# Kernel optimization log

Measured on AMD Instinct MI355X. Metric: run time of the kernel, lower is better.

The kernel has to match this reference:

```python
import jax, jax.numpy as jnp
import numpy as np

K = 8            # NEAREST_K
IN = 68          # input_size = 64 + 4
EO = 32          # edge_output_size
FEAT = IN * 2 + EO * 4  # 264
EMB = 32         # linear_embedding
NCLS = 2
N = 768
EPS = 1e-5


def lrelu(x):
    return jnp.where(x >= 0, x, 0.01 * x)


def setup_inputs() -> dict:
    key = jax.random.key(0)
    ks = jax.random.split(key, 16)

    def w(k, fan_in, fan_out):
        return jax.random.normal(k, (fan_in, fan_out), jnp.float32) / np.float32(np.sqrt(fan_in))

    return {
        "feat0": jax.random.normal(ks[0], (N, IN), jnp.float32),
        "feat1": jax.random.normal(ks[1], (N, IN), jnp.float32),
        # edge_conv1: Linear(IN*K, EO) -> LeakyReLU -> Linear(EO, EO) -> LeakyReLU
        "ec1_w1": w(ks[2], IN * K, EO), "ec1_b1": jnp.zeros((EO,), jnp.float32),
        "ec1_w2": w(ks[3], EO, EO),     "ec1_b2": jnp.zeros((EO,), jnp.float32),
        # edge_conv2: Linear(EO*K, EO) -> LeakyReLU -> Linear(EO, EO) -> LeakyReLU
        "ec2_w1": w(ks[4], EO * K, EO), "ec2_b1": jnp.zeros((EO,), jnp.float32),
        "ec2_w2": w(ks[5], EO, EO),     "ec2_b2": jnp.zeros((EO,), jnp.float32),
        # linear head: BN(FEAT) -> Linear(FEAT,EMB) -> LReLU -> Linear(EMB,EMB) -> LReLU -> Linear(EMB,NCLS)
        "bn_g": jnp.ones((FEAT,), jnp.float32), "bn_b": jnp.zeros((FEAT,), jnp.float32),
        "lin1_w": w(ks[6], FEAT, EMB), "lin1_b": jnp.zeros((EMB,), jnp.float32),
        "lin2_w": w(ks[7], EMB, EMB),  "lin2_b": jnp.zeros((EMB,), jnp.float32),
        "lin3_w": w(ks[8], EMB, NCLS), "lin3_b": jnp.zeros((NCLS,), jnp.float32),
    }


def _pairs_for_graph(feat, ec1_w1, ec1_b1, ec1_w2, ec1_b2,
                     ec2_w1, ec2_b1, ec2_w2, ec2_b2):
    n = feat.shape[0]
    # kNN on first 4 dims via pairwise L1 distance (includes self, dist 0)
    coords = feat[:, :4]
    dist = jnp.abs(coords[:, None, :] - coords[None, :, :]).sum(-1)  # [n, n]
    _, idx = jax.lax.top_k(-dist, K)  # [n, K] smallest distances

    # EdgeConv 1: gather neighbor features, flatten feature-major (matches torch transpose+view)
    e1 = feat[idx]                                  # [n, K, IN]
    e1 = jnp.swapaxes(e1, 1, 2).reshape(n, IN * K)  # [n, IN*K]
    e1 = lrelu(lrelu(e1 @ ec1_w1 + ec1_b1) @ ec1_w2 + ec1_b2)  # [n, EO]

    # EdgeConv 2 on edge1 outputs
    e2 = e1[idx]                                    # [n, K, EO]
    e2 = jnp.swapaxes(e2, 1, 2).reshape(n, EO * K)  # [n, EO*K]
    e2 = lrelu(lrelu(e2 @ ec2_w1 + ec2_b1) @ ec2_w2 + ec2_b2)  # [n, EO]

    x = jnp.concatenate([feat, e1, e2], axis=-1)    # [n, IN + 2*EO] = [n, 132]
    # upper-triangle (i<j) all-pairs concat, row-major order == torch masked_select of triu mask
    iu, ju = jnp.triu_indices(n, k=1)
    return jnp.concatenate([x[iu], x[ju]], axis=-1)  # [n(n-1)/2, FEAT]


def reference(feat0, feat1, ec1_w1, ec1_b1, ec1_w2, ec1_b2,
              ec2_w1, ec2_b1, ec2_w2, ec2_b2,
              bn_g, bn_b, lin1_w, lin1_b, lin2_w, lin2_b, lin3_w, lin3_b):
    ec = (ec1_w1, ec1_b1, ec1_w2, ec1_b2, ec2_w1, ec2_b1, ec2_w2, ec2_b2)
    x = jnp.concatenate([_pairs_for_graph(feat0, *ec),
                         _pairs_for_graph(feat1, *ec)], axis=0)  # [P, FEAT]
    # BatchNorm1d in training mode: batch statistics (biased variance)
    mu = x.mean(axis=0)
    var = x.var(axis=0)
    x = (x - mu) * jax.lax.rsqrt(var + EPS) * bn_g + bn_b
    x = lrelu(x @ lin1_w + lin1_b)
    x = lrelu(x @ lin2_w + lin2_b)
    return x @ lin3_w + lin3_b  # [P, NCLS]
```

## Files before the change

kernel.cpp:

```cpp
#include <hip/hip_runtime.h>

#define NN 768
#define IN_F 68
#define KNN 8
#define EO 32
#define FEAT 264
#define HALF_FEAT 132
#define EMB 32
#define NPAIR 294528

typedef __attribute__((ext_vector_type(8))) short bf16x8;
typedef __attribute__((ext_vector_type(4))) float f32x4;

static __device__ __forceinline__ int pack_chop2(float x0, float x1) {
  return __builtin_amdgcn_perm(__float_as_uint(x1), __float_as_uint(x0), 0x07060302);
}
static __device__ __forceinline__ float chop(float x) {
  return __uint_as_float(__float_as_uint(x) & 0xffff0000u);
}

__global__ void __launch_bounds__(64) topk_ec1_kernel(
    const float* __restrict__ feat0, const float* __restrict__ feat1,
    const float* __restrict__ w1, const float* __restrict__ b1,
    const float* __restrict__ w2, const float* __restrict__ b2,
    int* __restrict__ idx_out, float* __restrict__ e1out)
{
  const int i = blockIdx.x, g = blockIdx.y;
  const float* __restrict__ feat = g ? feat1 : feat0;
  const int lane = threadIdx.x;

  __shared__ unsigned long long keys[64*8];
  __shared__ int nbr[8];
  __shared__ float gl[KNN*IN_F];
  __shared__ float hsh[EO];

  const float4 ci = *(const float4*)(feat + i*IN_F);

  float4 cand[12];
#pragma unroll
  for (int t = 0; t < 12; t++)
    cand[t] = *(const float4*)(feat + (lane + 64*t)*IN_F);

  float bd[8]; int bidx[8];
#pragma unroll
  for (int k = 0; k < 8; k++) { bd[k] = 1e30f; bidx[k] = 0; }
#pragma unroll
  for (int t = 0; t < 12; t++) {
    const int j = lane + 64*t;
    float d = fabsf(ci.x - cand[t].x);
    d += fabsf(ci.y - cand[t].y);
    d += fabsf(ci.z - cand[t].z);
    d += fabsf(ci.w - cand[t].w);
    if (d < bd[7]) {
#pragma unroll
      for (int k = 7; k >= 1; k--) {
        if (d < bd[k-1])    { bd[k] = bd[k-1]; bidx[k] = bidx[k-1]; }
        else if (d < bd[k]) { bd[k] = d;       bidx[k] = j; }
      }
      if (d < bd[0]) { bd[0] = d; bidx[0] = j; }
    }
  }
#pragma unroll
  for (int k = 0; k < 8; k++)
    keys[lane*8+k] = ((unsigned long long)__float_as_uint(bd[k]) << 32) | (unsigned)bidx[k];
  __syncthreads();
  int pos = 0;
#pragma unroll
  for (int r = 0; r < 8; r++) {
    unsigned long long mykey = keys[lane*8 + pos];
    unsigned long long mn = mykey;
#pragma unroll
    for (int s = 32; s >= 1; s >>= 1) {
      unsigned long long o = __shfl_xor(mn, s, 64);
      mn = (o < mn) ? o : mn;
    }
    if (mykey == mn) pos++;
    if (lane == 0) {
      int nb = (int)(mn & 0xffffffffull);
      nbr[r] = nb;
      idx_out[(g*NN+i)*8 + r] = nb;
    }
  }
  __syncthreads();

  for (int z = lane; z < KNN*17; z += 64) {
    int k = z / 17, q = z - k*17;
    *(float4*)&gl[k*IN_F + q*4] = *(const float4*)(feat + nbr[k]*IN_F + q*4);
  }
  __syncthreads();

  const int e = lane & 31, hf = lane >> 5;
  float ak[8];
#pragma unroll
  for (int k = 0; k < 8; k++) ak[k] = 0.f;
  const int cbeg = hf*34;
  for (int c = cbeg; c < cbeg+34; c++) {
#pragma unroll
    for (int k = 0; k < 8; k++)
      ak[k] += gl[k*IN_F+c] * w1[(c*8+k)*EO + e];
  }
  float acc = ((ak[0]+ak[1])+(ak[2]+ak[3])) + ((ak[4]+ak[5])+(ak[6]+ak[7]));
  acc += __shfl_xor(acc, 32, 64);
  if (hf == 0) {
    float h = acc + b1[e];
    hsh[e] = fmaxf(h, 0.01f*h);
  }
  __syncthreads();
  if (lane < 32) {
    float o0=0.f, o1=0.f, o2=0.f, o3=0.f;
#pragma unroll
    for (int m = 0; m < 32; m += 4) {
      o0 += hsh[m+0] * w2[(m+0)*EO + lane];
      o1 += hsh[m+1] * w2[(m+1)*EO + lane];
      o2 += hsh[m+2] * w2[(m+2)*EO + lane];
      o3 += hsh[m+3] * w2[(m+3)*EO + lane];
    }
    float o = b2[lane] + ((o0+o1)+(o2+o3));
    o = fmaxf(o, 0.01f*o);
    e1out[(g*NN+i)*EO + lane] = o;
  }
}

__global__ void __launch_bounds__(64) ec2_kernel(
    const int* __restrict__ idx, const float* __restrict__ e1,
    const float* __restrict__ w1, const float* __restrict__ b1,
    const float* __restrict__ w2, const float* __restrict__ b2,
    float* __restrict__ e2out)
{
  const int i = blockIdx.x, g = blockIdx.y;
  const int lane = threadIdx.x;
  __shared__ float gl[KNN*EO];
  __shared__ float hsh[EO];
  {
    const int k = lane >> 3, q = lane & 7;
    const int nb = idx[(g*NN+i)*8 + k];
    *(float4*)&gl[k*EO + q*4] = *(const float4*)(e1 + (g*NN+nb)*EO + q*4);
  }
  __syncthreads();
  const int e = lane & 31, hf = lane >> 5;
  float ak[8];
#pragma unroll
  for (int k = 0; k < 8; k++) ak[k] = 0.f;
  const int cbeg = hf*16;
  for (int c = cbeg; c < cbeg+16; c++) {
#pragma unroll
    for (int k = 0; k < 8; k++)
      ak[k] += gl[k*EO+c] * w1[(c*8+k)*EO + e];
  }
  float acc = ((ak[0]+ak[1])+(ak[2]+ak[3])) + ((ak[4]+ak[5])+(ak[6]+ak[7]));
  acc += __shfl_xor(acc, 32, 64);
  if (hf == 0) {
    float h = acc + b1[e];
    hsh[e] = fmaxf(h, 0.01f*h);
  }
  __syncthreads();
  if (lane < 32) {
    float o0=0.f, o1=0.f, o2=0.f, o3=0.f;
#pragma unroll
    for (int m = 0; m < 32; m += 4) {
      o0 += hsh[m+0] * w2[(m+0)*EO + lane];
      o1 += hsh[m+1] * w2[(m+1)*EO + lane];
      o2 += hsh[m+2] * w2[(m+2)*EO + lane];
      o3 += hsh[m+3] * w2[(m+3)*EO + lane];
    }
    float o = b2[lane] + ((o0+o1)+(o2+o3));
    o = fmaxf(o, 0.01f*o);
    e2out[(g*NN+i)*EO + lane] = o;
  }
}

__global__ void __launch_bounds__(256) stats_kernel(
    const float* __restrict__ feat0, const float* __restrict__ feat1,
    const float* __restrict__ e1, const float* __restrict__ e2,
    const float* __restrict__ bn_g,
    float* __restrict__ mu_out, float* __restrict__ sg_out)
{
  const int c = blockIdx.x;
  const int tid = threadIdx.x;
  double s1=0, s2=0, q1=0, q2=0;
  for (int t = tid; t < 2*NN; t += 256) {
    int g = t >= NN;
    int i = t - g*NN;
    float val;
    if (c < IN_F)      val = (g ? feat1 : feat0)[i*IN_F + c];
    else if (c < 100)  val = e1[(g*NN+i)*EO + (c-IN_F)];
    else               val = e2[(g*NN+i)*EO + (c-100)];
    double dv = val;
    double wf = (double)(NN-1-i), wsnd = (double)i;
    s1 += wf*dv;  s2 += wsnd*dv;
    double dq = dv*dv;
    q1 += wf*dq;  q2 += wsnd*dq;
  }
#pragma unroll
  for (int off = 32; off >= 1; off >>= 1) {
    s1 += __shfl_xor(s1, off, 64);
    s2 += __shfl_xor(s2, off, 64);
    q1 += __shfl_xor(q1, off, 64);
    q2 += __shfl_xor(q2, off, 64);
  }
  __shared__ double red[4][4];
  const int w = tid >> 6;
  if ((tid & 63) == 0) { red[w][0]=s1; red[w][1]=s2; red[w][2]=q1; red[w][3]=q2; }
  __syncthreads();
  if (tid == 0) {
    double t0 = red[0][0]+red[1][0]+red[2][0]+red[3][0];
    double t1 = red[0][1]+red[1][1]+red[2][1]+red[3][1];
    double t2 = red[0][2]+red[1][2]+red[2][2]+red[3][2];
    double t3 = red[0][3]+red[1][3]+red[2][3]+red[3][3];
    const double M2 = 2.0 * (double)NPAIR;
    double mu1 = t0/M2, mu2 = t1/M2;
    double v1 = t2/M2 - mu1*mu1;
    double v2 = t3/M2 - mu2*mu2;
    mu_out[c]           = (float)mu1;
    mu_out[HALF_FEAT+c] = (float)mu2;
    sg_out[c]           = (float)((double)bn_g[c] / sqrt(v1 + 1e-5));
    sg_out[HALF_FEAT+c] = (float)((double)bn_g[HALF_FEAT+c] / sqrt(v2 + 1e-5));
  }
}

__global__ void __launch_bounds__(64) uv_c0_kernel(
    const float* __restrict__ feat0, const float* __restrict__ feat1,
    const float* __restrict__ e1, const float* __restrict__ e2,
    const float* __restrict__ sg, const float* __restrict__ mu,
    const float* __restrict__ bn_b,
    const float* __restrict__ lin1_w, const float* __restrict__ lin1_b,
    float* __restrict__ u, float* __restrict__ v, float* __restrict__ c0g)
{
  const int i = blockIdx.x, g = blockIdx.y;
  const int t = threadIdx.x;
  if (i == NN) {
    if (g == 0 && t < EMB) {
      float a0=0.f, a1=0.f, a2=0.f, a3=0.f;
      for (int c = 0; c < FEAT; c += 4) {
        a0 += (bn_b[c+0] - mu[c+0]*sg[c+0]) * lin1_w[(c+0)*EMB + t];
        a1 += (bn_b[c+1] - mu[c+1]*sg[c+1]) * lin1_w[(c+1)*EMB + t];
        a2 += (bn_b[c+2] - mu[c+2]*sg[c+2]) * lin1_w[(c+2)*EMB + t];
        a3 += (bn_b[c+3] - mu[c+3]*sg[c+3]) * lin1_w[(c+3)*EMB + t];
      }
      c0g[t] = lin1_b[t] + ((a0+a1)+(a2+a3));
    }
    return;
  }
  __shared__ float x[HALF_FEAT];
  for (int c = t; c < IN_F; c += 64) x[c] = (g ? feat1 : feat0)[i*IN_F + c];
  if (t < 32) x[IN_F + t]     = e1[(g*NN+i)*EO + t];
  else        x[100 + (t-32)] = e2[(g*NN+i)*EO + (t-32)];
  __syncthreads();
  const int e = t & 31, hf = t >> 5;
  const int base = hf * HALF_FEAT;
  float a0=0.f, a1=0.f, a2=0.f, a3=0.f;
  for (int c = 0; c < HALF_FEAT; c += 4) {
    a0 += x[c+0] * sg[base+c+0] * lin1_w[(base+c+0)*EMB + e];
    a1 += x[c+1] * sg[base+c+1] * lin1_w[(base+c+1)*EMB + e];
    a2 += x[c+2] * sg[base+c+2] * lin1_w[(base+c+2)*EMB + e];
    a3 += x[c+3] * sg[base+c+3] * lin1_w[(base+c+3)*EMB + e];
  }
  float acc = ((a0+a1)+(a2+a3));
  float* dst = hf ? v : u;
  dst[(g*NN+i)*EMB + e] = acc;
}

__global__ void __launch_bounds__(256) pair_kernel(
    const float* __restrict__ u, const float* __restrict__ v,
    const float* __restrict__ c0g,
    const float* __restrict__ lin2_w, const float* __restrict__ lin2_b,
    const float* __restrict__ lin3_w, const float* __restrict__ lin3_b,
    float2* __restrict__ out)
{
  const int g = blockIdx.y;
  int rem = blockIdx.x;
  int a = 0;
  while (rem >= 48 - a) { rem -= 48 - a; a++; }
  const int b = a + rem;

  __shared__ float su[16*36], sv[16*36];
  __shared__ float wbuf[4][16*36];
  const int tid = threadIdx.x;
  {
    int r = tid >> 5, c = tid & 31;
    su[r*36+c] = u[(g*NN + a*16 + r)*EMB + c];
    sv[r*36+c] = v[(g*NN + b*16 + r)*EMB + c];
    r += 8;
    su[r*36+c] = u[(g*NN + a*16 + r)*EMB + c];
    sv[r*36+c] = v[(g*NN + b*16 + r)*EMB + c];
  }
  __syncthreads();

  const int lane = tid & 63, w = tid >> 6;
  const int q = lane & 15, kg = lane >> 4;

  union { int i[4]; bf16x8 v; } whi0, wlo0, whi1, wlo1;
#pragma unroll
  for (int d = 0; d < 4; d++) {
    float w0a = lin2_w[(kg*8+2*d)*32 + q],      w0b = lin2_w[(kg*8+2*d+1)*32 + q];
    float w1a = lin2_w[(kg*8+2*d)*32 + 16 + q], w1b = lin2_w[(kg*8+2*d+1)*32 + 16 + q];
    whi0.i[d] = pack_chop2(w0a, w0b);
    wlo0.i[d] = pack_chop2(w0a - chop(w0a), w0b - chop(w0b));
    whi1.i[d] = pack_chop2(w1a, w1b);
    wlo1.i[d] = pack_chop2(w1a - chop(w1a), w1b - chop(w1b));
  }
  float svc[8];
#pragma unroll
  for (int jj = 0; jj < 8; jj++)
    svc[jj] = sv[q*36 + kg*8 + jj] + c0g[kg*8+jj];
  float2 w3v[8]; float b2v[8];
#pragma unroll
  for (int jj = 0; jj < 8; jj++) {
    w3v[jj] = ((const float2*)lin3_w)[kg*8+jj];
    b2v[jj] = lin2_b[kg*8+jj];
  }
  const float b30 = lin3_b[0], b31 = lin3_b[1];

  float* wb = wbuf[w];
#pragma unroll
  for (int t = 0; t < 4; t++) {
    const int ty = w*4 + t;
    const float4 sa = *(const float4*)&su[ty*36 + kg*8];
    const float4 sb = *(const float4*)&su[ty*36 + kg*8 + 4];
    float se[8] = {sa.x, sa.y, sa.z, sa.w, sb.x, sb.y, sb.z, sb.w};
    union { int i[4]; bf16x8 v; } ahi, alo;
#pragma unroll
    for (int d = 0; d < 4; d++) {
      float s0 = se[2*d]   + svc[2*d];
      float s1 = se[2*d+1] + svc[2*d+1];
      s0 = fmaxf(s0, 0.01f*s0);
      s1 = fmaxf(s1, 0.01f*s1);
      ahi.i[d] = pack_chop2(s0, s1);
      alo.i[d] = pack_chop2(s0 - chop(s0), s1 - chop(s1));
    }
    f32x4 acc0 = {0.f,0.f,0.f,0.f}, acc1 = {0.f,0.f,0.f,0.f};
    acc0 = __builtin_amdgcn_mfma_f32_16x16x32_bf16(ahi.v, whi0.v, acc0, 0,0,0);
    acc1 = __builtin_amdgcn_mfma_f32_16x16x32_bf16(ahi.v, whi1.v, acc1, 0,0,0);
    acc0 = __builtin_amdgcn_mfma_f32_16x16x32_bf16(ahi.v, wlo0.v, acc0, 0,0,0);
    acc1 = __builtin_amdgcn_mfma_f32_16x16x32_bf16(ahi.v, wlo1.v, acc1, 0,0,0);
    acc0 = __builtin_amdgcn_mfma_f32_16x16x32_bf16(alo.v, whi0.v, acc0, 0,0,0);
    acc1 = __builtin_amdgcn_mfma_f32_16x16x32_bf16(alo.v, whi1.v, acc1, 0,0,0);
#pragma unroll
    for (int r = 0; r < 4; r++) {
      wb[(kg*4+r)*36 + q]      = acc0[r];
      wb[(kg*4+r)*36 + 16 + q] = acc1[r];
    }
    float o0 = 0.f, o1 = 0.f;
#pragma unroll
    for (int jj = 0; jj < 8; jj++) {
      float h = wb[q*36 + kg*8 + jj] + b2v[jj];
      h = fmaxf(h, 0.01f*h);
      o0 += h * w3v[jj].x;
      o1 += h * w3v[jj].y;
    }
    o0 += __shfl_xor(o0, 16, 64); o0 += __shfl_xor(o0, 32, 64);
    o1 += __shfl_xor(o1, 16, 64); o1 += __shfl_xor(o1, 32, 64);
    const int i = a*16 + ty, j = b*16 + q;
    if (lane < 16 && j > i) {
      long p = (long)i*NN - (long)i*(i+1)/2 + (j - i - 1);
      out[(long)g*NPAIR + p] = make_float2(o0 + b30, o1 + b31);
    }
  }
}

extern "C" void kernel_launch(void* const* d_in, const int* in_sizes, int n_in,
                              void* d_out, int out_size, void* d_ws, size_t ws_size,
                              hipStream_t stream)
{
  const float* feat0  = (const float*)d_in[0];
  const float* feat1  = (const float*)d_in[1];
  const float* ec1_w1 = (const float*)d_in[2];
  const float* ec1_b1 = (const float*)d_in[3];
  const float* ec1_w2 = (const float*)d_in[4];
  const float* ec1_b2 = (const float*)d_in[5];
  const float* ec2_w1 = (const float*)d_in[6];
  const float* ec2_b1 = (const float*)d_in[7];
  const float* ec2_w2 = (const float*)d_in[8];
  const float* ec2_b2 = (const float*)d_in[9];
  const float* bn_g   = (const float*)d_in[10];
  const float* bn_b   = (const float*)d_in[11];
  const float* lin1_w = (const float*)d_in[12];
  const float* lin1_b = (const float*)d_in[13];
  const float* lin2_w = (const float*)d_in[14];
  const float* lin2_b = (const float*)d_in[15];
  const float* lin3_w = (const float*)d_in[16];
  const float* lin3_b = (const float*)d_in[17];

  char* ws = (char*)d_ws;
  int*   idx = (int*)  (ws + 0);
  float* e1  = (float*)(ws + 49152);
  float* e2  = (float*)(ws + 245760);
  float* u   = (float*)(ws + 442368);
  float* v   = (float*)(ws + 638976);
  float* mu  = (float*)(ws + 835584);
  float* sg  = (float*)(ws + 836640);
  float* c0g = (float*)(ws + 837696);

  topk_ec1_kernel<<<dim3(768,2), 64, 0, stream>>>(feat0, feat1, ec1_w1, ec1_b1,
                                                  ec1_w2, ec1_b2, idx, e1);
  ec2_kernel<<<dim3(768,2), 64, 0, stream>>>(idx, e1, ec2_w1, ec2_b1,
                                             ec2_w2, ec2_b2, e2);
  stats_kernel<<<dim3(132), 256, 0, stream>>>(feat0, feat1, e1, e2, bn_g, mu, sg);
  uv_c0_kernel<<<dim3(769,2), 64, 0, stream>>>(feat0, feat1, e1, e2, sg, mu, bn_b,
                                               lin1_w, lin1_b, u, v, c0g);
  pair_kernel<<<dim3(1176,2), 256, 0, stream>>>(u, v, c0g, lin2_w, lin2_b,
                                                lin3_w, lin3_b, (float2*)d_out);
}
```

Baseline: 137.6 us.

## Fuse BN statistics into edge-conv kernels via fixed-point atomics and last-block finalize

Drops the separate stats kernel. The edge-conv kernels now accumulate the weighted sums and sums of squares per channel with 64-bit fixed-point global atomics, and the last block to finish (found with an atomic counter) computes mu, scale and c0. The goal is to remove one kernel launch and a serial reduction pass, and to shrink the uv kernel by taking out its extra c0 block. In exchange it adds many atomics per row (four per channel) and fixed-point quantization of the statistics, and the result now depends on global counters being reset correctly between calls.

```diff
diff --git a/kernel.cpp b/kernel.cpp
--- a/kernel.cpp
+++ b/kernel.cpp
@@ -17,6 +17,24 @@
 }
 static __device__ __forceinline__ float chop(float x) {
   return __uint_as_float(__float_as_uint(x) & 0xffff0000u);
+}
+
+#define SL 16777216.0
+#define SQ 65536.0
+
+__device__ long long g_T0[HALF_FEAT];
+__device__ long long g_T1[HALF_FEAT];
+__device__ long long g_Q0[HALF_FEAT];
+__device__ long long g_Q1[HALF_FEAT];
+__device__ unsigned  g_done;
+
+static __device__ __forceinline__ void stat_add(int c, int i, float v) {
+  long long iq = __double2ll_rn((double)v * SL);
+  long long qq = __double2ll_rn((double)v * (double)v * SQ);
+  __hip_atomic_fetch_add(&g_T0[c], iq, __ATOMIC_RELAXED, __HIP_MEMORY_SCOPE_AGENT);
+  __hip_atomic_fetch_add(&g_T1[c], (long long)i * iq, __ATOMIC_RELAXED, __HIP_MEMORY_SCOPE_AGENT);
+  __hip_atomic_fetch_add(&g_Q0[c], qq, __ATOMIC_RELAXED, __HIP_MEMORY_SCOPE_AGENT);
+  __hip_atomic_fetch_add(&g_Q1[c], (long long)i * qq, __ATOMIC_RELAXED, __HIP_MEMORY_SCOPE_AGENT);
 }
 
 __global__ void __launch_bounds__(64) topk_ec1_kernel(
@@ -118,19 +136,28 @@
     float o = b2[lane] + ((o0+o1)+(o2+o3));
     o = fmaxf(o, 0.01f*o);
     e1out[(g*NN+i)*EO + lane] = o;
-  }
+    stat_add(IN_F + lane, i, o);
+  }
+  for (int z = lane; z < IN_F; z += 64)
+    stat_add(z, i, feat[i*IN_F + z]);
 }
 
 __global__ void __launch_bounds__(64) ec2_kernel(
     const int* __restrict__ idx, const float* __restrict__ e1,
     const float* __restrict__ w1, const float* __restrict__ b1,
     const float* __restrict__ w2, const float* __restrict__ b2,
-    float* __restrict__ e2out)
+    const float* __restrict__ bn_g, const float* __restrict__ bn_b,
+    const float* __restrict__ lin1_w, const float* __restrict__ lin1_b,
+    float* __restrict__ e2out,
+    float* __restrict__ mu_out, float* __restrict__ sg_out,
+    float* __restrict__ c0g)
 {
   const int i = blockIdx.x, g = blockIdx.y;
   const int lane = threadIdx.x;
   __shared__ float gl[KNN*EO];
   __shared__ float hsh[EO];
+  __shared__ float smu[FEAT], ssg[FEAT];
+  __shared__ int isLast;
   {
     const int k = lane >> 3, q = lane & 7;
     const int nb = idx[(g*NN+i)*8 + k];
@@ -166,81 +193,67 @@
     float o = b2[lane] + ((o0+o1)+(o2+o3));
     o = fmaxf(o, 0.01f*o);
     e2out[(g*NN+i)*EO + lane] = o;
-  }
-}
-
-__global__ void __launch_bounds__(256) stats_kernel(
+    stat_add(100 + lane, i, o);
+  }
+
+  asm volatile("s_waitcnt vmcnt(0)" ::: "memory");
+  if (lane == 0) {
+    unsigned old = __hip_atomic_fetch_add(&g_done, 1u,
+                     __ATOMIC_RELAXED, __HIP_MEMORY_SCOPE_AGENT);
+    isLast = (old == 2u*NN - 1u);
+  }
+  __syncthreads();
+  if (!isLast) return;
+
+  for (int c = lane; c < HALF_FEAT; c += 64) {
+    long long T0 = __hip_atomic_load(&g_T0[c], __ATOMIC_RELAXED, __HIP_MEMORY_SCOPE_AGENT);
+    long long T1 = __hip_atomic_load(&g_T1[c], __ATOMIC_RELAXED, __HIP_MEMORY_SCOPE_AGENT);
+    long long Q0 = __hip_atomic_load(&g_Q0[c], __ATOMIC_RELAXED, __HIP_MEMORY_SCOPE_AGENT);
+    long long Q1 = __hip_atomic_load(&g_Q1[c], __ATOMIC_RELAXED, __HIP_MEMORY_SCOPE_AGENT);
+    __hip_atomic_store(&g_T0[c], 0ll, __ATOMIC_RELAXED, __HIP_MEMORY_SCOPE_AGENT);
+    __hip_atomic_store(&g_T1[c], 0ll, __ATOMIC_RELAXED, __HIP_MEMORY_SCOPE_AGENT);
+    __hip_atomic_store(&g_Q0[c], 0ll, __ATOMIC_RELAXED, __HIP_MEMORY_SCOPE_AGENT);
+    __hip_atomic_store(&g_Q1[c], 0ll, __ATOMIC_RELAXED, __HIP_MEMORY_SCOPE_AGENT);
+    const double M2 = 2.0 * (double)NPAIR;
+    double s1 = (double)((long long)(NN-1)*T0 - T1) * (1.0/SL);
+    double s2 = (double)T1 * (1.0/SL);
+    double q1 = (double)((long long)(NN-1)*Q0 - Q1) * (1.0/SQ);
+    double q2 = (double)Q1 * (1.0/SQ);
+    double mu1 = s1/M2, mu2 = s2/M2;
+    double v1 = q1/M2 - mu1*mu1;
+    double v2 = q2/M2 - mu2*mu2;
+    float m1 = (float)mu1, m2 = (float)mu2;
+    float g1 = (float)((double)bn_g[c] / sqrt(v1 + 1e-5));
+    float g2 = (float)((double)bn_g[HALF_FEAT+c] / sqrt(v2 + 1e-5));
+    mu_out[c] = m1;  mu_out[HALF_FEAT+c] = m2;
+    sg_out[c] = g1;  sg_out[HALF_FEAT+c] = g2;
+    smu[c] = m1;  smu[HALF_FEAT+c] = m2;
+    ssg[c] = g1;  ssg[HALF_FEAT+c] = g2;
+  }
+  if (lane == 0)
+    __hip_atomic_store(&g_done, 0u, __ATOMIC_RELAXED, __HIP_MEMORY_SCOPE_AGENT);
+  __syncthreads();
+  if (lane < EMB) {
+    float a0=0.f, a1=0.f, a2=0.f, a3=0.f;
+    for (int c = 0; c < FEAT; c += 4) {
+      a0 += (bn_b[c+0] - smu[c+0]*ssg[c+0]) * lin1_w[(c+0)*EMB + lane];
+      a1 += (bn_b[c+1] - smu[c+1]*ssg[c+1]) * lin1_w[(c+1)*EMB + lane];
+      a2 += (bn_b[c+2] - smu[c+2]*ssg[c+2]) * lin1_w[(c+2)*EMB + lane];
+      a3 += (bn_b[c+3] - smu[c+3]*ssg[c+3]) * lin1_w[(c+3)*EMB + lane];
+    }
+    c0g[lane] = lin1_b[lane] + ((a0+a1)+(a2+a3));
+  }
+}
+
+__global__ void __launch_bounds__(64) uv_kernel(
     const float* __restrict__ feat0, const float* __restrict__ feat1,
     const float* __restrict__ e1, const float* __restrict__ e2,
-    const float* __restrict__ bn_g,
-    float* __restrict__ mu_out, float* __restrict__ sg_out)
-{
-  const int c = blockIdx.x;
-  const int tid = threadIdx.x;
-  double s1=0, s2=0, q1=0, q2=0;
-  for (int t = tid; t < 2*NN; t += 256) {
-    int g = t >= NN;
-    int i = t - g*NN;
-    float val;
-    if (c < IN_F)      val = (g ? feat1 : feat0)[i*IN_F + c];
-    else if (c < 100)  val = e1[(g*NN+i)*EO + (c-IN_F)];
-    else               val = e2[(g*NN+i)*EO + (c-100)];
-    double dv = val;
-    double wf = (double)(NN-1-i), wsnd = (double)i;
-    s1 += wf*dv;  s2 += wsnd*dv;
-    double dq = dv*dv;
-    q1 += wf*dq;  q2 += wsnd*dq;
-  }
-#pragma unroll
-  for (int off = 32; off >= 1; off >>= 1) {
-    s1 += __shfl_xor(s1, off, 64);
-    s2 += __shfl_xor(s2, off, 64);
-    q1 += __shfl_xor(q1, off, 64);
-    q2 += __shfl_xor(q2, off, 64);
-  }
-  __shared__ double red[4][4];
-  const int w = tid >> 6;
-  if ((tid & 63) == 0) { red[w][0]=s1; red[w][1]=s2; red[w][2]=q1; red[w][3]=q2; }
-  __syncthreads();
-  if (tid == 0) {
-    double t0 = red[0][0]+red[1][0]+red[2][0]+red[3][0];
-    double t1 = red[0][1]+red[1][1]+red[2][1]+red[3][1];
-    double t2 = red[0][2]+red[1][2]+red[2][2]+red[3][2];
-    double t3 = red[0][3]+red[1][3]+red[2][3]+red[3][3];
-    const double M2 = 2.0 * (double)NPAIR;
-    double mu1 = t0/M2, mu2 = t1/M2;
-    double v1 = t2/M2 - mu1*mu1;
-    double v2 = t3/M2 - mu2*mu2;
-    mu_out[c]           = (float)mu1;
-    mu_out[HALF_FEAT+c] = (float)mu2;
-    sg_out[c]           = (float)((double)bn_g[c] / sqrt(v1 + 1e-5));
-    sg_out[HALF_FEAT+c] = (float)((double)bn_g[HALF_FEAT+c] / sqrt(v2 + 1e-5));
-  }
-}
-
-__global__ void __launch_bounds__(64) uv_c0_kernel(
-    const float* __restrict__ feat0, const float* __restrict__ feat1,
-    const float* __restrict__ e1, const float* __restrict__ e2,
-    const float* __restrict__ sg, const float* __restrict__ mu,
-    const float* __restrict__ bn_b,
-    const float* __restrict__ lin1_w, const float* __restrict__ lin1_b,
-    float* __restrict__ u, float* __restrict__ v, float* __restrict__ c0g)
+    const float* __restrict__ sg,
+    const float* __restrict__ lin1_w,
+    float* __restrict__ u, float* __restrict__ v)
 {
   const int i = blockIdx.x, g = blockIdx.y;
   const int t = threadIdx.x;
-  if (i == NN) {
-    if (g == 0 && t < EMB) {
-      float a0=0.f, a1=0.f, a2=0.f, a3=0.f;
-      for (int c = 0; c < FEAT; c += 4) {
-        a0 += (bn_b[c+0] - mu[c+0]*sg[c+0]) * lin1_w[(c+0)*EMB + t];
-        a1 += (bn_b[c+1] - mu[c+1]*sg[c+1]) * lin1_w[(c+1)*EMB + t];
-        a2 += (bn_b[c+2] - mu[c+2]*sg[c+2]) * lin1_w[(c+2)*EMB + t];
-        a3 += (bn_b[c+3] - mu[c+3]*sg[c+3]) * lin1_w[(c+3)*EMB + t];
-      }
-      c0g[t] = lin1_b[t] + ((a0+a1)+(a2+a3));
-    }
-    return;
-  }
   __shared__ float x[HALF_FEAT];
   for (int c = t; c < IN_F; c += 64) x[c] = (g ? feat1 : feat0)[i*IN_F + c];
   if (t < 32) x[IN_F + t]     = e1[(g*NN+i)*EO + t];
@@ -292,8 +305,10 @@
   union { int i[4]; bf16x8 v; } whi0, wlo0, whi1, wlo1;
 #pragma unroll
   for (int d = 0; d < 4; d++) {
-    float w0a = lin2_w[(kg*8+2*d)*32 + q],      w0b = lin2_w[(kg*8+2*d+1)*32 + q];
-    float w1a = lin2_w[(kg*8+2*d)*32 + 16 + q], w1b = lin2_w[(kg*8+2*d+1)*32 + 16 + q];
+    float w0a = lin2_w[(kg*8+2*d)*32 + q];
+    float w0b = lin2_w[(kg*8+2*d+1)*32 + q];
+    float w1a = lin2_w[(kg*8+2*d)*32 + 16 + q];
+    float w1b = lin2_w[(kg*8+2*d+1)*32 + 16 + q];
     whi0.i[d] = pack_chop2(w0a, w0b);
     wlo0.i[d] = pack_chop2(w0a - chop(w0a), w0b - chop(w0b));
     whi1.i[d] = pack_chop2(w1a, w1b);
@@ -394,10 +409,10 @@
   topk_ec1_kernel<<<dim3(768,2), 64, 0, stream>>>(feat0, feat1, ec1_w1, ec1_b1,
                                                   ec1_w2, ec1_b2, idx, e1);
   ec2_kernel<<<dim3(768,2), 64, 0, stream>>>(idx, e1, ec2_w1, ec2_b1,
-                                             ec2_w2, ec2_b2, e2);
-  stats_kernel<<<dim3(132), 256, 0, stream>>>(feat0, feat1, e1, e2, bn_g, mu, sg);
-  uv_c0_kernel<<<dim3(769,2), 64, 0, stream>>>(feat0, feat1, e1, e2, sg, mu, bn_b,
-                                               lin1_w, lin1_b, u, v, c0g);
+                                             ec2_w2, ec2_b2, bn_g, bn_b,
+                                             lin1_w, lin1_b, e2, mu, sg, c0g);
+  uv_kernel<<<dim3(768,2), 64, 0, stream>>>(feat0, feat1, e1, e2, sg,
+                                            lin1_w, u, v);
   pair_kernel<<<dim3(1176,2), 256, 0, stream>>>(u, v, c0g, lin2_w, lin2_b,
                                                 lin3_w, lin3_b, (float2*)d_out);
 }
```

Measured after the change: 240.6 us. +74.9%, slower.

## Split topk_ec1 work across two waves per block

Applied to the files above, without the earlier changes.

The kNN + EdgeConv1 kernel now launches 128 threads per row instead of 64. Each wave scans half the candidates and then one wave merges the two sets of per-lane sorted lists. The EC1 first-layer dot products are split by neighbor across the two waves, and the second layer is split across four 32-thread groups, with partial sums combined through shared memory. The aim is to shorten the per-block serial latency of this kernel, at the cost of extra barriers and shared-memory reductions.

```diff
diff --git a/kernel.cpp b/kernel.cpp
--- a/kernel.cpp
+++ b/kernel.cpp
@@ -19,7 +19,8 @@
   return __uint_as_float(__float_as_uint(x) & 0xffff0000u);
 }
 
-__global__ void __launch_bounds__(64) topk_ec1_kernel(
+
+__global__ void __launch_bounds__(128) topk_ec1_kernel(
     const float* __restrict__ feat0, const float* __restrict__ feat1,
     const float* __restrict__ w1, const float* __restrict__ b1,
     const float* __restrict__ w2, const float* __restrict__ b2,
@@ -27,26 +28,29 @@
 {
   const int i = blockIdx.x, g = blockIdx.y;
   const float* __restrict__ feat = g ? feat1 : feat0;
-  const int lane = threadIdx.x;
-
-  __shared__ unsigned long long keys[64*8];
+  const int tid = threadIdx.x;
+  const int lane = tid & 63, wv = tid >> 6;
+
+  __shared__ unsigned long long keys[128*8];
   __shared__ int nbr[8];
   __shared__ float gl[KNN*IN_F];
   __shared__ float hsh[EO];
+  __shared__ float part1[2][EO];
+  __shared__ float part2[4][EO];
 
   const float4 ci = *(const float4*)(feat + i*IN_F);
 
-  float4 cand[12];
-#pragma unroll
-  for (int t = 0; t < 12; t++)
-    cand[t] = *(const float4*)(feat + (lane + 64*t)*IN_F);
+  float4 cand[6];
+#pragma unroll
+  for (int t = 0; t < 6; t++)
+    cand[t] = *(const float4*)(feat + (tid + 128*t)*IN_F);
 
   float bd[8]; int bidx[8];
 #pragma unroll
   for (int k = 0; k < 8; k++) { bd[k] = 1e30f; bidx[k] = 0; }
 #pragma unroll
-  for (int t = 0; t < 12; t++) {
-    const int j = lane + 64*t;
+  for (int t = 0; t < 6; t++) {
+    const int j = tid + 128*t;
     float d = fabsf(ci.x - cand[t].x);
     d += fabsf(ci.y - cand[t].y);
     d += fabsf(ci.z - cand[t].z);
@@ -62,62 +66,77 @@
   }
 #pragma unroll
   for (int k = 0; k < 8; k++)
-    keys[lane*8+k] = ((unsigned long long)__float_as_uint(bd[k]) << 32) | (unsigned)bidx[k];
-  __syncthreads();
-  int pos = 0;
-#pragma unroll
-  for (int r = 0; r < 8; r++) {
-    unsigned long long mykey = keys[lane*8 + pos];
-    unsigned long long mn = mykey;
-#pragma unroll
-    for (int s = 32; s >= 1; s >>= 1) {
-      unsigned long long o = __shfl_xor(mn, s, 64);
-      mn = (o < mn) ? o : mn;
-    }
-    if (mykey == mn) pos++;
-    if (lane == 0) {
-      int nb = (int)(mn & 0xffffffffull);
-      nbr[r] = nb;
-      idx_out[(g*NN+i)*8 + r] = nb;
-    }
-  }
-  __syncthreads();
-
-  for (int z = lane; z < KNN*17; z += 64) {
+    keys[tid*8+k] = ((unsigned long long)__float_as_uint(bd[k]) << 32) | (unsigned)bidx[k];
+  __syncthreads();
+
+  if (wv == 0) {
+    int posA = 0, posB = 0;
+#pragma unroll
+    for (int r = 0; r < 8; r++) {
+      unsigned long long ha = keys[lane*8 + posA];
+      unsigned long long hb = keys[(lane+64)*8 + posB];
+      unsigned long long mn = ha < hb ? ha : hb;
+#pragma unroll
+      for (int s = 32; s >= 1; s >>= 1) {
+        unsigned long long o = __shfl_xor(mn, s, 64);
+        mn = (o < mn) ? o : mn;
+      }
+      if (ha == mn) posA++;
+      else if (hb == mn) posB++;
+      if (lane == 0) {
+        int nb = (int)(mn & 0xffffffffull);
+        nbr[r] = nb;
+        idx_out[(g*NN+i)*8 + r] = nb;
+      }
+    }
+  }
+  __syncthreads();
+
+  for (int z = tid; z < KNN*17; z += 128) {
     int k = z / 17, q = z - k*17;
     *(float4*)&gl[k*IN_F + q*4] = *(const float4*)(feat + nbr[k]*IN_F + q*4);
   }
   __syncthreads();
 
   const int e = lane & 31, hf = lane >> 5;
-  float ak[8];
-#pragma unroll
-  for (int k = 0; k < 8; k++) ak[k] = 0.f;
+  float ak[4];
+#pragma unroll
+  for (int k = 0; k < 4; k++) ak[k] = 0.f;
   const int cbeg = hf*34;
+  const int kbase = wv*4;
   for (int c = cbeg; c < cbeg+34; c++) {
 #pragma unroll
-    for (int k = 0; k < 8; k++)
-      ak[k] += gl[k*IN_F+c] * w1[(c*8+k)*EO + e];
-  }
-  float acc = ((ak[0]+ak[1])+(ak[2]+ak[3])) + ((ak[4]+ak[5])+(ak[6]+ak[7]));
+    for (int k = 0; k < 4; k++)
+      ak[k] += gl[(kbase+k)*IN_F+c] * w1[(c*8+kbase+k)*EO + e];
+  }
+  float acc = (ak[0]+ak[1])+(ak[2]+ak[3]);
   acc += __shfl_xor(acc, 32, 64);
-  if (hf == 0) {
-    float h = acc + b1[e];
-    hsh[e] = fmaxf(h, 0.01f*h);
-  }
-  __syncthreads();
-  if (lane < 32) {
+  if (hf == 0) part1[wv][e] = acc;
+  __syncthreads();
+  if (tid < 32) {
+    float h = part1[0][tid] + part1[1][tid] + b1[tid];
+    hsh[tid] = fmaxf(h, 0.01f*h);
+  }
+  __syncthreads();
+
+  const int qq = tid >> 5, ee = tid & 31;
+  {
     float o0=0.f, o1=0.f, o2=0.f, o3=0.f;
-#pragma unroll
-    for (int m = 0; m < 32; m += 4) {
-      o0 += hsh[m+0] * w2[(m+0)*EO + lane];
-      o1 += hsh[m+1] * w2[(m+1)*EO + lane];
-      o2 += hsh[m+2] * w2[(m+2)*EO + lane];
-      o3 += hsh[m+3] * w2[(m+3)*EO + lane];
-    }
-    float o = b2[lane] + ((o0+o1)+(o2+o3));
+    const int mbeg = qq*8;
+#pragma unroll
+    for (int m = mbeg; m < mbeg+8; m += 4) {
+      o0 += hsh[m+0] * w2[(m+0)*EO + ee];
+      o1 += hsh[m+1] * w2[(m+1)*EO + ee];
+      o2 += hsh[m+2] * w2[(m+2)*EO + ee];
+      o3 += hsh[m+3] * w2[(m+3)*EO + ee];
+    }
+    part2[qq][ee] = ((o0+o1)+(o2+o3));
+  }
+  __syncthreads();
+  if (tid < 32) {
+    float o = b2[tid] + ((part2[0][tid]+part2[1][tid])+(part2[2][tid]+part2[3][tid]));
     o = fmaxf(o, 0.01f*o);
-    e1out[(g*NN+i)*EO + lane] = o;
+    e1out[(g*NN+i)*EO + tid] = o;
   }
 }
 
@@ -292,8 +311,10 @@
   union { int i[4]; bf16x8 v; } whi0, wlo0, whi1, wlo1;
 #pragma unroll
   for (int d = 0; d < 4; d++) {
-    float w0a = lin2_w[(kg*8+2*d)*32 + q],      w0b = lin2_w[(kg*8+2*d+1)*32 + q];
-    float w1a = lin2_w[(kg*8+2*d)*32 + 16 + q], w1b = lin2_w[(kg*8+2*d+1)*32 + 16 + q];
+    float w0a = lin2_w[(kg*8+2*d)*32 + q];
+    float w0b = lin2_w[(kg*8+2*d+1)*32 + q];
+    float w1a = lin2_w[(kg*8+2*d)*32 + 16 + q];
+    float w1b = lin2_w[(kg*8+2*d+1)*32 + 16 + q];
     whi0.i[d] = pack_chop2(w0a, w0b);
     wlo0.i[d] = pack_chop2(w0a - chop(w0a), w0b - chop(w0b));
     whi1.i[d] = pack_chop2(w1a, w1b);
@@ -391,8 +412,8 @@
   float* sg  = (float*)(ws + 836640);
   float* c0g = (float*)(ws + 837696);
 
-  topk_ec1_kernel<<<dim3(768,2), 64, 0, stream>>>(feat0, feat1, ec1_w1, ec1_b1,
-                                                  ec1_w2, ec1_b2, idx, e1);
+  topk_ec1_kernel<<<dim3(768,2), 128, 0, stream>>>(feat0, feat1, ec1_w1, ec1_b1,
+                                                   ec1_w2, ec1_b2, idx, e1);
   ec2_kernel<<<dim3(768,2), 64, 0, stream>>>(idx, e1, ec2_w1, ec2_b1,
                                              ec2_w2, ec2_b2, e2);
   stats_kernel<<<dim3(132), 256, 0, stream>>>(feat0, feat1, e1, e2, bn_g, mu, sg);
```

New measurement: 134.4 us. 2.3% less time.
